# Performance work log

Hardware: AMD Instinct MI355X
Metric: run time of the kernel (lower is better)

## Reference

```python
import jax, jax.numpy as jnp
import numpy as np

E, S, L, V, PMAX = 256, 64, 3, 256, 2000
DILATIONS = (1, 2, 4, 8)


def _layernorm(x, g, b, eps=1e-5):
    m = x.mean(-1, keepdims=True)
    v = ((x - m) ** 2).mean(-1, keepdims=True)
    return (x - m) * jax.lax.rsqrt(v + eps) * g + b


def _ssm_layer(x, in_w, conv_w, conv_b, dt_w, A_log, D_param, B_w, C_w, out_w, ln_g, ln_b):
    # x: [B, T, D]
    Bsz, T, Dm = x.shape
    xr = x @ in_w.T                                  # [B,T,2D]
    x_in, x_res = xr[..., :Dm], xr[..., Dm:]
    # causal depthwise conv, kernel=4, left-pad 3 (== torch pad=3 then [:, :, :T])
    xt = x_in.transpose(0, 2, 1)                     # [B,D,T]
    xc = jax.lax.conv_general_dilated(
        xt, conv_w[:, None, :], (1,), [(3, 0)],
        feature_group_count=Dm, dimension_numbers=('NCH', 'OIH', 'NCH'))
    xc = jax.nn.silu((xc + conv_b[None, :, None]).transpose(0, 2, 1))  # [B,T,D]
    A = -jnp.exp(A_log)                              # [D,S]
    Bm = xc @ B_w.T                                  # [B,T,S]
    Cm = xc @ C_w.T                                  # [B,T,S]
    dt = jax.nn.softplus(dt_w)                       # [D] per-channel timestep
    dA = 1.0 + dt[:, None] * A                       # Euler discretization I + dt*A, [D,S]
    h0 = jnp.zeros((Bsz, Dm, S), x.dtype)

    def step(h, inp):
        u_t, B_t, C_t = inp                          # [B,D],[B,S],[B,S]
        h = dA * h + (dt * u_t)[:, :, None] * B_t[:, None, :]   # [B,D,S]
        y = jnp.einsum('bs,bds->bd', C_t, h)
        return h, y

    _, ys = jax.lax.scan(step, h0, (xc.transpose(1, 0, 2), Bm.transpose(1, 0, 2), Cm.transpose(1, 0, 2)))
    y = ys.transpose(1, 0, 2) + D_param * xc         # [B,T,D]
    y = (y * jax.nn.silu(x_res)) @ out_w.T
    return _layernorm(y + x, ln_g, ln_b)


def _forward(tokens, tok_emb, pos_emb, in_w, conv_w, conv_b, dt_w, A_log, D_param,
             B_w, C_w, out_w, ln_g, ln_b, ctx_w, ctx_b, fus_w, fus_b, fus_ln_g, fus_ln_b):
    Bsz, T = tokens.shape
    x = tok_emb[tokens] + pos_emb[:T][None]          # [B,T,E]
    feats = x
    for i in range(L):
        feats = _ssm_layer(feats, in_w[i], conv_w[i], conv_b[i], dt_w[i], A_log[i],
                           D_param[i], B_w[i], C_w[i], out_w[i], ln_g[i], ln_b[i])
    # multi-dilation context convs on the raw embeddings
    xt = x.transpose(0, 2, 1)                        # [B,E,T]
    ctx = []
    for j, d in enumerate(DILATIONS):
        o = jax.lax.conv_general_dilated(
            xt, ctx_w[j], (1,), [(d, d)], rhs_dilation=(d,),
            dimension_numbers=('NCH', 'OIH', 'NCH'))
        ctx.append(o + ctx_b[j][None, :, None])
    ctx = jnp.concatenate(ctx, axis=1).transpose(0, 2, 1)      # [B,T,E]
    fused = jax.nn.relu(jnp.concatenate([feats, ctx], -1) @ fus_w.T + fus_b)
    return _layernorm(fused, fus_ln_g, fus_ln_b)


def setup_inputs() -> dict:
    key = jax.random.key(0)
    ks = jax.random.split(key, 16)
    Bsz, T = 32, 2000

    def n(k, shape, s):
        return jax.random.normal(k, shape, jnp.float32) * s

    return {
        'tokens': jax.random.randint(ks[0], (Bsz, T), 0, V),
        'tok_emb': n(ks[1], (V, E), 1.0),
        'pos_emb': n(ks[2], (PMAX, E), 1.0),
        'in_w': n(ks[3], (L, 2 * E, E), 0.05),
        'conv_w': n(ks[4], (L, E, 4), 0.2),
        'conv_b': jnp.zeros((L, E), jnp.float32),
        'dt_w': jax.random.uniform(ks[5], (L, E), jnp.float32, -0.01, 0.01),
        'A_log': jax.random.uniform(ks[6], (L, E, S), jnp.float32, -4.0, -1.0),
        'D_param': jnp.zeros((L, E), jnp.float32),
        'B_w': n(ks[7], (L, S, E), 0.05),
        'C_w': n(ks[8], (L, S, E), 0.05),
        'out_w': n(ks[9], (L, E, E), 0.05),
        'ln_g': jnp.ones((L, E), jnp.float32),
        'ln_b': jnp.zeros((L, E), jnp.float32),
        'ctx_w': n(ks[10], (4, E // 4, E, 3), 0.05),
        'ctx_b': jnp.zeros((4, E // 4), jnp.float32),
        'fus_w': n(ks[11], (E, 2 * E), 0.05),
        'fus_b': jnp.zeros((E,), jnp.float32),
        'fus_ln_g': jnp.ones((E,), jnp.float32),
        'fus_ln_b': jnp.zeros((E,), jnp.float32),
    }


def reference(tokens, tok_emb, pos_emb, in_w, conv_w, conv_b, dt_w, A_log, D_param,
              B_w, C_w, out_w, ln_g, ln_b, ctx_w, ctx_b, fus_w, fus_b, fus_ln_g, fus_ln_b):
    return _forward(tokens, tok_emb, pos_emb, in_w, conv_w, conv_b, dt_w, A_log, D_param,
                    B_w, C_w, out_w, ln_g, ln_b, ctx_w, ctx_b, fus_w, fus_b, fus_ln_g, fus_ln_b)
```

## Files before the change

### kernel.cpp

```cpp
#include <hip/hip_runtime.h>
#include <stdint.h>

#define B_ 32
#define T_ 2000
#define E_ 256
#define S_ 64
#define L_ 3
#define BT_ (B_*T_)
#define NC_ 16
#define CL_ 125
#define TP_ (T_+16)

typedef short s8v __attribute__((ext_vector_type(8)));
typedef short s4v __attribute__((ext_vector_type(4)));
typedef float f4v __attribute__((ext_vector_type(4)));
typedef unsigned short us;

__device__ __forceinline__ float b2f(us u){
    return __uint_as_float(((unsigned int)u) << 16);
}
__device__ __forceinline__ us f2b(float f){
    unsigned int x = __float_as_uint(f);
    x += 0x7fffu + ((x >> 16) & 1u);
    return (us)(x >> 16);
}

__global__ __launch_bounds__(256) void cvtw_k(const float* __restrict__ src,
    us* __restrict__ dst)
{
    int idx = blockIdx.x*256 + threadIdx.x;
    f4v v = *(const f4v*)(src + (size_t)idx*4);
    s4v o;
    #pragma unroll
    for (int j=0;j<4;j++) o[j] = (short)f2b(v[j]);
    *(s4v*)(dst + (size_t)idx*4) = o;
}

__global__ __launch_bounds__(256) void packw_k(const float* __restrict__ cw,
    us* __restrict__ wp)
{
    int idx = blockIdx.x*256 + threadIdx.x;
    int i2 = idx % 768; int r = idx / 768;
    int c = r & 63; int j = r >> 6;
    int tap = i2 >> 8; int i = i2 & 255;
    wp[idx] = f2b(cw[(((size_t)(j*64 + c))*E_ + i)*3 + tap]);
}

__global__ __launch_bounds__(256) void embed_k(const int* __restrict__ tok,
    const float* __restrict__ te, const float* __restrict__ pe, us* __restrict__ x0)
{
    int idx = blockIdx.x*256 + threadIdx.x;
    int dg = idx & 31; int bt = idx >> 5; int t = bt % T_;
    int tk = tok[bt] & 255;
    const float* ta = te + (size_t)tk*E_ + dg*8;
    const float* pa = pe + (size_t)t*E_ + dg*8;
    f4v a0 = *(const f4v*)ta, a1 = *(const f4v*)(ta+4);
    f4v p0 = *(const f4v*)pa, p1 = *(const f4v*)(pa+4);
    s8v o;
    #pragma unroll
    for (int j=0;j<4;j++){
        o[j]   = (short)f2b(a0[j] + p0[j]);
        o[j+4] = (short)f2b(a1[j] + p1[j]);
    }
    *(s8v*)(x0 + (size_t)bt*E_ + dg*8) = o;
}

__global__ __launch_bounds__(256) void lconst_k(const float* __restrict__ dt_w,
    const float* __restrict__ A_log, float* __restrict__ dtv,
    float* __restrict__ dAT, float* __restrict__ dApT)
{
    int idx = blockIdx.x*256 + threadIdx.x;
    int d = idx & (E_-1); int s = idx >> 8;
    float dt = log1pf(expf(dt_w[d]));
    float A  = -expf(A_log[d*S_ + s]);
    float dA = 1.f + dt*A;
    dAT[s*E_ + d]  = dA;
    dApT[s*E_ + d] = powf(dA, (float)CL_);
    if (s == 0) dtv[d] = dt;
}

__global__ __launch_bounds__(256) void dwconv_k(const us* __restrict__ xin,
    const float* __restrict__ cw, const float* __restrict__ cb, us* __restrict__ xc)
{
    int idx = blockIdx.x*256 + threadIdx.x;
    int dg = idx & 31; int bt = idx >> 5; int t = bt % T_;
    int d0 = dg*8;
    float acc[8]; float w[8][4];
    #pragma unroll
    for (int j=0;j<8;j++){
        f4v wv = *(const f4v*)(cw + (size_t)(d0+j)*4);
        #pragma unroll
        for (int k=0;k<4;k++) w[j][k] = wv[k];
        acc[j] = cb[d0+j];
    }
    #pragma unroll
    for (int k=0;k<4;k++){
        if (t + k - 3 >= 0){
            s8v xv = *(const s8v*)(xin + (size_t)(bt + k - 3)*E_ + d0);
            #pragma unroll
            for (int j=0;j<8;j++) acc[j] = fmaf(b2f((us)xv[j]), w[j][k], acc[j]);
        }
    }
    s8v o;
    #pragma unroll
    for (int j=0;j<8;j++){ float v = acc[j]; v = v / (1.f + expf(-v)); o[j] = (short)f2b(v); }
    *(s8v*)(xc + (size_t)bt*E_ + d0) = o;
}

#define BM 128
#define BN 64
#define BK 32

template<int AMODE, int EPI>
__global__ __launch_bounds__(256)
void gemm_k(const us* __restrict__ A1, const us* __restrict__ A2,
            int lda, int shift,
            const us* __restrict__ W, int ldw,
            void* __restrict__ C1, const float* __restrict__ bias,
            int ldc, int K)
{
    __shared__ us Al[BM*BK];
    __shared__ us Bl[BN*BK];
    const int tid = threadIdx.x;
    const int wid = tid >> 6, lane = tid & 63;
    const int m0 = blockIdx.x * BM;
    const int n0 = blockIdx.y * BN;
    const int wr = wid >> 1, wc = wid & 1;
    f4v acc[4][2];
    #pragma unroll
    for (int a=0;a<4;a++)
        #pragma unroll
        for (int b=0;b<2;b++) acc[a][b] = (f4v){0.f,0.f,0.f,0.f};

    for (int k0 = 0; k0 < K; k0 += BK){
        s8v va[2], vb;
        #pragma unroll
        for (int i=0;i<2;i++){
            int g = i*256 + tid;
            int row = g >> 2, ks = g & 3;
            const us* src;
            if constexpr (AMODE==0){
                src = A1 + (size_t)(m0+row)*lda + k0 + ks*8;
            } else if constexpr (AMODE==2){
                int kk = k0 + ks*8;
                const us* base = (kk < E_) ? A1 : A2;
                src = base + (size_t)(m0+row)*E_ + (kk & (E_-1));
            } else {
                int kk = k0 + ks*8;
                int tap = kk >> 8; int kin = kk & (E_-1);
                int m = m0 + row; int bb = m / T_; int tt = m - bb*T_;
                src = A1 + ((size_t)bb*TP_ + 8 + tt + (tap-1)*shift)*E_ + kin;
            }
            va[i] = *(const s8v*)src;
        }
        {
            int row = tid >> 2, ks = tid & 3;
            vb = *(const s8v*)(W + (size_t)(n0+row)*ldw + k0 + ks*8);
        }
        if (k0) __syncthreads();
        #pragma unroll
        for (int i=0;i<2;i++) *(s8v*)(Al + (size_t)(i*256 + tid)*8) = va[i];
        *(s8v*)(Bl + (size_t)tid*8) = vb;
        __syncthreads();

        s8v af[4], bfr[2];
        #pragma unroll
        for (int mr=0;mr<4;mr++)
            af[mr] = *(const s8v*)(Al + ((size_t)(wr*64 + mr*16 + (lane&15))*4 + (lane>>4))*8);
        #pragma unroll
        for (int nr=0;nr<2;nr++)
            bfr[nr] = *(const s8v*)(Bl + ((size_t)(wc*32 + nr*16 + (lane&15))*4 + (lane>>4))*8);
        #pragma unroll
        for (int mr=0;mr<4;mr++)
            #pragma unroll
            for (int nr=0;nr<2;nr++)
                acc[mr][nr] = __builtin_amdgcn_mfma_f32_16x16x32_bf16(af[mr], bfr[nr], acc[mr][nr], 0, 0, 0);
    }
    #pragma unroll
    for (int mr=0;mr<4;mr++){
        #pragma unroll
        for (int nr=0;nr<2;nr++){
            int col = n0 + wc*32 + nr*16 + (lane & 15);
            int rb  = m0 + wr*64 + mr*16 + ((lane >> 4) << 2);
            #pragma unroll
            for (int i=0;i<4;i++){
                float val = acc[mr][nr][i];
                size_t row = (size_t)(rb + i);
                if constexpr (EPI==0){
                    ((us*)C1)[row*ldc + col] = f2b(val);
                } else if constexpr (EPI==5){
                    val += bias[col];
                    ((us*)C1)[row*ldc + col] = f2b(val);
                } else {
                    val += bias[col];
                    val = fmaxf(val, 0.f);
                    ((float*)C1)[row*ldc + col] = val;
                }
            }
        }
    }
}

__global__ __launch_bounds__(256) void scan_local(
    const float* __restrict__ dAT, const float* __restrict__ dtv,
    const us* __restrict__ xc, const us* __restrict__ Bm, const us* __restrict__ Cm,
    us* __restrict__ ys, us* __restrict__ H)
{
    int b = blockIdx.x >> 4, c = blockIdx.x & (NC_-1);
    int d = threadIdx.x;
    float h[S_], dAr[S_];
    #pragma unroll
    for (int s=0;s<S_;s++){ h[s]=0.f; dAr[s]=dAT[s*E_+d]; }
    float dtd = dtv[d];
    int t0 = c*CL_;
    for (int t=t0; t<t0+CL_; ++t){
        size_t bt = (size_t)b*T_ + t;
        float ku = dtd * b2f(xc[bt*E_ + d]);
        const s8v* Bp = (const s8v*)(Bm + bt*S_);
        const s8v* Cp = (const s8v*)(Cm + bt*S_);
        float y = 0.f;
        #pragma unroll
        for (int s8=0;s8<S_/8;s8++){
            s8v bv = Bp[s8], cv = Cp[s8];
            #pragma unroll
            for (int j=0;j<8;j++){
                int s = s8*8+j;
                h[s] = fmaf(dAr[s], h[s], ku*b2f((us)bv[j]));
                y    = fmaf(b2f((us)cv[j]), h[s], y);
            }
        }
        ys[bt*E_ + d] = f2b(y);
    }
    size_t hb = ((size_t)(b*NC_ + c))*S_*E_ + d;
    #pragma unroll
    for (int s=0;s<S_;s++) H[hb + (size_t)s*E_] = f2b(h[s]);
}

__global__ __launch_bounds__(256) void carry_k(const float* __restrict__ dApT,
    us* H)
{
    int idx = blockIdx.x*256 + threadIdx.x;
    int d = idx & (E_-1); int s = (idx >> 8) & (S_-1); int b = idx >> 14;
    float ap = dApT[s*E_ + d];
    size_t base = ((size_t)(b*NC_))*S_*E_ + (size_t)s*E_ + d;
    float hh = 0.f;
    for (int c=0;c<NC_;c++){
        size_t p = base + (size_t)c*S_*E_;
        float hl = b2f(H[p]);
        H[p] = f2b(hh);
        hh = fmaf(ap, hh, hl);
    }
}

__global__ __launch_bounds__(256) void scan_fix(
    const float* __restrict__ dAT, const us* __restrict__ H,
    const us* __restrict__ Cm, us* ys)
{
    int b = blockIdx.x / (NC_-1); int c = 1 + blockIdx.x % (NC_-1);
    int d = threadIdx.x;
    float w[S_], dAr[S_];
    size_t cb = ((size_t)(b*NC_ + c))*S_*E_ + d;
    #pragma unroll
    for (int s=0;s<S_;s++){ dAr[s] = dAT[s*E_+d]; w[s] = dAr[s]*b2f(H[cb + (size_t)s*E_]); }
    int t0 = c*CL_;
    for (int t=t0; t<t0+CL_; ++t){
        size_t bt = (size_t)b*T_ + t;
        const s8v* Cp = (const s8v*)(Cm + bt*S_);
        float y = 0.f;
        #pragma unroll
        for (int s8=0;s8<S_/8;s8++){
            s8v cv = Cp[s8];
            #pragma unroll
            for (int j=0;j<8;j++){
                int s = s8*8+j;
                y = fmaf(b2f((us)cv[j]), w[s], y);
                w[s] *= dAr[s];
            }
        }
        size_t p = bt*E_ + d;
        ys[p] = f2b(b2f(ys[p]) + y);
    }
}

__global__ __launch_bounds__(256) void zin_k(const us* __restrict__ ys,
    const us* xc, const us* __restrict__ xres,
    const float* __restrict__ Dp, us* zout)
{
    size_t e0 = ((size_t)blockIdx.x*256 + threadIdx.x)*4;
    int d0 = (int)(e0 & (E_-1));
    s4v yv  = *(const s4v*)(ys + e0);
    s4v xcv = *(const s4v*)(xc + e0);
    s4v xrv = *(const s4v*)(xres + e0);
    f4v dv  = *(const f4v*)(Dp + d0);
    s4v o;
    #pragma unroll
    for (int j=0;j<4;j++){
        float y  = b2f((us)yv[j]) + dv[j] * b2f((us)xcv[j]);
        float xr = b2f((us)xrv[j]);
        o[j] = (short)f2b(y * (xr / (1.f + expf(-xr))));
    }
    *(s4v*)(zout + e0) = o;
}

__global__ __launch_bounds__(256) void ln_k(const us* z,
    const us* __restrict__ resid, const float* __restrict__ g,
    const float* __restrict__ bb, us* out)
{
    int wid = threadIdx.x >> 6, lane = threadIdx.x & 63;
    size_t row = (size_t)blockIdx.x*4 + wid;
    size_t base = row*E_ + lane*4;
    s4v zv = *(const s4v*)(z + base);
    float v[4];
    #pragma unroll
    for (int j=0;j<4;j++) v[j] = b2f((us)zv[j]);
    if (resid){
        s4v rv = *(const s4v*)(resid + base);
        #pragma unroll
        for (int j=0;j<4;j++) v[j] += b2f((us)rv[j]);
    }
    float sum = v[0]+v[1]+v[2]+v[3];
    float sq  = v[0]*v[0]+v[1]*v[1]+v[2]*v[2]+v[3]*v[3];
    #pragma unroll
    for (int off=32; off>0; off>>=1){
        sum += __shfl_xor(sum, off, 64);
        sq  += __shfl_xor(sq,  off, 64);
    }
    float mean = sum * (1.f/E_);
    float var  = sq * (1.f/E_) - mean*mean;
    float rstd = rsqrtf(var + 1e-5f);
    f4v gv = *(const f4v*)(g + lane*4);
    f4v bv = *(const f4v*)(bb + lane*4);
    s4v o;
    #pragma unroll
    for (int j=0;j<4;j++)
        o[j] = (short)f2b((v[j]-mean)*rstd*gv[j] + bv[j]);
    *(s4v*)(out + base) = o;
}

__global__ __launch_bounds__(256) void ln_f32_k(const float* z,
    const float* __restrict__ g, const float* __restrict__ bb, float* out)
{
    int wid = threadIdx.x >> 6, lane = threadIdx.x & 63;
    size_t row = (size_t)blockIdx.x*4 + wid;
    size_t base = row*E_ + lane*4;
    f4v v = *(const f4v*)(z + base);
    float sum = v[0]+v[1]+v[2]+v[3];
    float sq  = v[0]*v[0]+v[1]*v[1]+v[2]*v[2]+v[3]*v[3];
    #pragma unroll
    for (int off=32; off>0; off>>=1){
        sum += __shfl_xor(sum, off, 64);
        sq  += __shfl_xor(sq,  off, 64);
    }
    float mean = sum * (1.f/E_);
    float var  = sq * (1.f/E_) - mean*mean;
    float rstd = rsqrtf(var + 1e-5f);
    f4v gv = *(const f4v*)(g + lane*4);
    f4v bv = *(const f4v*)(bb + lane*4);
    f4v o;
    #pragma unroll
    for (int j=0;j<4;j++)
        o[j] = (v[j]-mean)*rstd*gv[j] + bv[j];
    *(f4v*)(out + base) = o;
}

__global__ __launch_bounds__(256) void xpad_k(const us* __restrict__ x0,
    us* __restrict__ xp)
{
    int idx = blockIdx.x*256 + threadIdx.x;
    int dg = idx & 31; int r = idx >> 5;
    int tp = r % TP_; int b = r / TP_;
    s8v o;
    if (tp < 8 || tp >= T_+8){
        #pragma unroll
        for (int j=0;j<8;j++) o[j] = 0;
    } else {
        o = *(const s8v*)(x0 + ((size_t)b*T_ + tp - 8)*E_ + dg*8);
    }
    *(s8v*)(xp + (size_t)r*E_ + dg*8) = o;
}

__global__ void probe_k(const unsigned int* __restrict__ outw,
    const us* p0, const us* bm, const us* ctxb, const us* p1, const us* xc,
    const float* temb, float* outf)
{
    if (threadIdx.x | blockIdx.x) return;
    bool zero = true;
    for (int i=0;i<512 && zero;i++)              if (outw[i]) zero = false;
    for (int i=2000000;i<2000512 && zero;i++)    if (outw[i]) zero = false;
    if (!zero) return;
    int code = 256, f;
    f=0; for (int i=0;i<256;i++) if (p0[i]   & 0x7FFF) f=1;  code += 128*f;
    f=0; for (int i=0;i<256;i++) if (bm[i]   & 0x7FFF) f=1;  code += 64*f;
    f=0; for (int i=0;i<256;i++) if (ctxb[i] & 0x7FFF) f=1;  code += 32*f;
    f=0; for (int i=0;i<256;i++) if (p1[i]   & 0x7FFF) f=1;  code += 16*f;
    f=0; for (int i=0;i<256;i++) if (xc[i]   & 0x7FFF) f=1;  code += 8*f;
    f=1; for (int i=0;i<64;i++){ float v = fabsf(temb[i]); if (!(v < 1024.f)) f=0; }
    code += 4*f;
    outf[0] = (float)code;
}

extern "C" void kernel_launch(void* const* d_in, const int* in_sizes, int n_in,
                              void* d_out, int out_size, void* d_ws, size_t ws_size,
                              hipStream_t stream)
{
    const int*   tokens   = (const int*)d_in[0];
    const float* tok_emb  = (const float*)d_in[1];
    const float* pos_emb  = (const float*)d_in[2];
    const float* in_w     = (const float*)d_in[3];
    const float* conv_w   = (const float*)d_in[4];
    const float* conv_b   = (const float*)d_in[5];
    const float* dt_w     = (const float*)d_in[6];
    const float* A_log    = (const float*)d_in[7];
    const float* D_param  = (const float*)d_in[8];
    const float* B_w      = (const float*)d_in[9];
    const float* C_w      = (const float*)d_in[10];
    const float* out_w    = (const float*)d_in[11];
    const float* ln_g     = (const float*)d_in[12];
    const float* ln_b     = (const float*)d_in[13];
    const float* ctx_w    = (const float*)d_in[14];
    const float* ctx_b    = (const float*)d_in[15];
    const float* fus_w    = (const float*)d_in[16];
    const float* fus_b    = (const float*)d_in[17];
    const float* fus_ln_g = (const float*)d_in[18];
    const float* fus_ln_b = (const float*)d_in[19];

    char* ws = (char*)d_ws;
    size_t off = 0;
    auto alloc = [&](size_t bytes){ size_t o = off; off += (bytes + 255) & ~(size_t)255; return o; };
    const size_t BT = BT_;
    size_t o_p0  = alloc(BT*E_*2);
    size_t o_p1  = alloc(BT*E_*2);
    size_t o_ctx = alloc(BT*E_*2);
    size_t o_xin = alloc(BT*E_*2);
    size_t o_xc  = alloc(BT*E_*2);
    size_t o_bm  = alloc(BT*S_*2);
    size_t o_cm  = alloc(BT*S_*2);
    size_t o_h   = alloc((size_t)B_*NC_*S_*E_*2);
    size_t o_wp  = alloc((size_t)4*64*768*2);
    size_t o_wi  = alloc((size_t)L_*2*E_*E_*2);
    size_t o_wo  = alloc((size_t)L_*E_*E_*2);
    size_t o_wb  = alloc((size_t)L_*S_*E_*2);
    size_t o_wc  = alloc((size_t)L_*S_*E_*2);
    size_t o_wf  = alloc((size_t)E_*2*E_*2);
    size_t o_dtv = alloc(E_*4);
    size_t o_dat = alloc(E_*S_*4);
    size_t o_dap = alloc(E_*S_*4);
    (void)ws_size; (void)in_sizes; (void)n_in; (void)out_size;

    us* P0   = (us*)(ws + o_p0);
    us* P1   = (us*)(ws + o_p1);
    us* CTXB = (us*)(ws + o_ctx);
    us* XIN  = (us*)(ws + o_xin);
    us* XC   = (us*)(ws + o_xc);
    us* Bm   = (us*)(ws + o_bm);
    us* Cm   = (us*)(ws + o_cm);
    us* Hb   = (us*)(ws + o_h);
    us* WP   = (us*)(ws + o_wp);
    us* WI   = (us*)(ws + o_wi);
    us* WO   = (us*)(ws + o_wo);
    us* WB   = (us*)(ws + o_wb);
    us* WC   = (us*)(ws + o_wc);
    us* WF   = (us*)(ws + o_wf);
    float* DTV  = (float*)(ws + o_dtv);
    float* DAT  = (float*)(ws + o_dat);
    float* DAPT = (float*)(ws + o_dap);
    us* XPAD = XIN;
    us* YS   = (us*)d_out;

    cvtw_k<<<L_*2*E_*E_/1024, 256, 0, stream>>>(in_w,  WI);
    cvtw_k<<<L_*E_*E_/1024,   256, 0, stream>>>(out_w, WO);
    cvtw_k<<<L_*S_*E_/1024,   256, 0, stream>>>(B_w,   WB);
    cvtw_k<<<L_*S_*E_/1024,   256, 0, stream>>>(C_w,   WC);
    cvtw_k<<<E_*2*E_/1024,    256, 0, stream>>>(fus_w, WF);
    packw_k<<<4*64*768/256,   256, 0, stream>>>(ctx_w, WP);

    embed_k<<<BT_*32/256, 256, 0, stream>>>(tokens, tok_emb, pos_emb, P0);

    xpad_k<<<B_*TP_*32/256, 256, 0, stream>>>(P0, XPAD);
    const int dil[4] = {1,2,4,8};
    for (int j = 0; j < 4; ++j){
        gemm_k<3,5><<<dim3(BT_/BM, 1), 256, 0, stream>>>(
            XPAD, nullptr, E_, dil[j], WP + (size_t)j*64*768, 768,
            CTXB + j*64, ctx_b + j*64, E_, 768);
    }

    for (int l = 0; l < L_; ++l){
        const us* xprev = (l==1) ? P1 : P0;
        us*       xnext = (l==1) ? P0 : P1;

        lconst_k<<<E_*S_/256, 256, 0, stream>>>(dt_w + (size_t)l*E_, A_log + (size_t)l*E_*S_,
                                                DTV, DAT, DAPT);
        gemm_k<0,0><<<dim3(BT_/BM, E_/BN), 256, 0, stream>>>(
            xprev, nullptr, E_, 0, WI + (size_t)l*2*E_*E_, E_, XIN, nullptr, E_, E_);
        dwconv_k<<<BT_*32/256, 256, 0, stream>>>(XIN, conv_w + (size_t)l*E_*4, conv_b + (size_t)l*E_, XC);
        gemm_k<0,0><<<dim3(BT_/BM, E_/BN), 256, 0, stream>>>(
            xprev, nullptr, E_, 0, WI + (size_t)l*2*E_*E_ + (size_t)E_*E_, E_, XIN , nullptr, E_, E_);
        gemm_k<0,0><<<dim3(BT_/BM, 1), 256, 0, stream>>>(
            XC, nullptr, E_, 0, WB + (size_t)l*S_*E_, E_, Bm, nullptr, S_, E_);
        gemm_k<0,0><<<dim3(BT_/BM, 1), 256, 0, stream>>>(
            XC, nullptr, E_, 0, WC + (size_t)l*S_*E_, E_, Cm, nullptr, S_, E_);
        scan_local<<<B_*NC_, 256, 0, stream>>>(DAT, DTV, XC, Bm, Cm, YS, Hb);
        carry_k<<<B_*S_*E_/256, 256, 0, stream>>>(DAPT, Hb);
        scan_fix<<<B_*(NC_-1), 256, 0, stream>>>(DAT, Hb, Cm, YS);
        zin_k<<<BT_*E_/4/256, 256, 0, stream>>>(YS, XC, XIN, D_param + (size_t)l*E_, XC );
        gemm_k<0,0><<<dim3(BT_/BM, E_/BN), 256, 0, stream>>>(
            XC, nullptr, E_, 0, WO + (size_t)l*E_*E_, E_, XIN , nullptr, E_, E_);
        ln_k<<<BT_/4, 256, 0, stream>>>(XIN, xprev, ln_g + (size_t)l*E_, ln_b + (size_t)l*E_, xnext);
    }

    gemm_k<2,6><<<dim3(BT_/BM, E_/BN), 256, 0, stream>>>(
        P1, CTXB, E_, 0, WF, 2*E_, d_out, fus_b, E_, 2*E_);
    ln_f32_k<<<BT_/4, 256, 0, stream>>>((const float*)d_out, fus_ln_g, fus_ln_b, (float*)d_out);

    probe_k<<<1, 64, 0, stream>>>((const unsigned int*)d_out, P0, Bm, CTXB, P1, XC,
                                  tok_emb, (float*)d_out);
}
```

Baseline: 1.475 ms.

## Split SSM scan state across four lanes per channel and store B/C in fp32

The chunked scan kernels now give each channel four threads, each holding 16 of the 64 state entries, and combine partial outputs with lane shuffles. This launches four times as many blocks and cuts per-thread register arrays from 128 to 32 floats, aiming for higher occupancy in the sequential scan. The B and C projection GEMMs now write fp32 instead of bf16, which removes unpacking in the scan but doubles their memory traffic. The probe kernel is trimmed to match the changed buffers.

New measurement: 2.823 ms. +91.4%, slower.

```diff
diff --git a/kernel.cpp b/kernel.cpp
--- a/kernel.cpp
+++ b/kernel.cpp
@@ -188,6 +188,8 @@
                 size_t row = (size_t)(rb + i);
                 if constexpr (EPI==0){
                     ((us*)C1)[row*ldc + col] = f2b(val);
+                } else if constexpr (EPI==2){
+                    ((float*)C1)[row*ldc + col] = val;
                 } else if constexpr (EPI==5){
                     val += bias[col];
                     ((us*)C1)[row*ldc + col] = f2b(val);
@@ -203,37 +205,45 @@
 
 __global__ __launch_bounds__(256) void scan_local(
     const float* __restrict__ dAT, const float* __restrict__ dtv,
-    const us* __restrict__ xc, const us* __restrict__ Bm, const us* __restrict__ Cm,
+    const us* __restrict__ xc, const float* __restrict__ Bm, const float* __restrict__ Cm,
     us* __restrict__ ys, us* __restrict__ H)
 {
-    int b = blockIdx.x >> 4, c = blockIdx.x & (NC_-1);
-    int d = threadIdx.x;
-    float h[S_], dAr[S_];
-    #pragma unroll
-    for (int s=0;s<S_;s++){ h[s]=0.f; dAr[s]=dAT[s*E_+d]; }
+    int blk = blockIdx.x;
+    int dq = blk & 3;
+    int c  = (blk >> 2) & (NC_-1);
+    int b  = blk >> 6;
+    int tid = threadIdx.x;
+    int dl = tid >> 2, sg = tid & 3;
+    int d  = dq*64 + dl;
+    int s0 = sg*16;
+    float h[16], dAr[16];
+    #pragma unroll
+    for (int j=0;j<16;j++){ h[j]=0.f; dAr[j]=dAT[(s0+j)*E_ + d]; }
     float dtd = dtv[d];
     int t0 = c*CL_;
     for (int t=t0; t<t0+CL_; ++t){
         size_t bt = (size_t)b*T_ + t;
-        float ku = dtd * b2f(xc[bt*E_ + d]);
-        const s8v* Bp = (const s8v*)(Bm + bt*S_);
-        const s8v* Cp = (const s8v*)(Cm + bt*S_);
+        float u = dtd * b2f(xc[bt*E_ + d]);
+        const f4v* Bp = (const f4v*)(Bm + bt*S_ + s0);
+        const f4v* Cp = (const f4v*)(Cm + bt*S_ + s0);
         float y = 0.f;
         #pragma unroll
-        for (int s8=0;s8<S_/8;s8++){
-            s8v bv = Bp[s8], cv = Cp[s8];
+        for (int q=0;q<4;q++){
+            f4v bv = Bp[q], cv = Cp[q];
             #pragma unroll
-            for (int j=0;j<8;j++){
-                int s = s8*8+j;
-                h[s] = fmaf(dAr[s], h[s], ku*b2f((us)bv[j]));
-                y    = fmaf(b2f((us)cv[j]), h[s], y);
+            for (int j=0;j<4;j++){
+                int s = q*4+j;
+                h[s] = fmaf(dAr[s], h[s], u*bv[j]);
+                y    = fmaf(cv[j], h[s], y);
             }
         }
-        ys[bt*E_ + d] = f2b(y);
+        y += __shfl_xor(y, 1, 64);
+        y += __shfl_xor(y, 2, 64);
+        if (sg == 0) ys[bt*E_ + d] = f2b(y);
     }
     size_t hb = ((size_t)(b*NC_ + c))*S_*E_ + d;
     #pragma unroll
-    for (int s=0;s<S_;s++) H[hb + (size_t)s*E_] = f2b(h[s]);
+    for (int j=0;j<16;j++) H[hb + (size_t)(s0+j)*E_] = f2b(h[j]);
 }
 
 __global__ __launch_bounds__(256) void carry_k(const float* __restrict__ dApT,
@@ -254,31 +264,45 @@
 
 __global__ __launch_bounds__(256) void scan_fix(
     const float* __restrict__ dAT, const us* __restrict__ H,
-    const us* __restrict__ Cm, us* ys)
-{
-    int b = blockIdx.x / (NC_-1); int c = 1 + blockIdx.x % (NC_-1);
-    int d = threadIdx.x;
-    float w[S_], dAr[S_];
+    const float* __restrict__ Cm, us* ys)
+{
+    int blk = blockIdx.x;
+    int dq = blk & 3;
+    int r  = blk >> 2;
+    int c  = 1 + r % (NC_-1);
+    int b  = r / (NC_-1);
+    int tid = threadIdx.x;
+    int dl = tid >> 2, sg = tid & 3;
+    int d  = dq*64 + dl;
+    int s0 = sg*16;
+    float w[16], dAr[16];
     size_t cb = ((size_t)(b*NC_ + c))*S_*E_ + d;
     #pragma unroll
-    for (int s=0;s<S_;s++){ dAr[s] = dAT[s*E_+d]; w[s] = dAr[s]*b2f(H[cb + (size_t)s*E_]); }
+    for (int j=0;j<16;j++){
+        dAr[j] = dAT[(s0+j)*E_ + d];
+        w[j]   = dAr[j]*b2f(H[cb + (size_t)(s0+j)*E_]);
+    }
     int t0 = c*CL_;
     for (int t=t0; t<t0+CL_; ++t){
         size_t bt = (size_t)b*T_ + t;
-        const s8v* Cp = (const s8v*)(Cm + bt*S_);
+        const f4v* Cp = (const f4v*)(Cm + bt*S_ + s0);
         float y = 0.f;
         #pragma unroll
-        for (int s8=0;s8<S_/8;s8++){
-            s8v cv = Cp[s8];
+        for (int q=0;q<4;q++){
+            f4v cv = Cp[q];
             #pragma unroll
-            for (int j=0;j<8;j++){
-                int s = s8*8+j;
-                y = fmaf(b2f((us)cv[j]), w[s], y);
+            for (int j=0;j<4;j++){
+                int s = q*4+j;
+                y = fmaf(cv[j], w[s], y);
                 w[s] *= dAr[s];
             }
         }
-        size_t p = bt*E_ + d;
-        ys[p] = f2b(b2f(ys[p]) + y);
+        y += __shfl_xor(y, 1, 64);
+        y += __shfl_xor(y, 2, 64);
+        if (sg == 0){
+            size_t p = bt*E_ + d;
+            ys[p] = f2b(b2f(ys[p]) + y);
+        }
     }
 }
 
@@ -380,8 +404,7 @@
 }
 
 __global__ void probe_k(const unsigned int* __restrict__ outw,
-    const us* p0, const us* bm, const us* ctxb, const us* p1, const us* xc,
-    const float* temb, float* outf)
+    const us* p0, const us* p1, float* outf)
 {
     if (threadIdx.x | blockIdx.x) return;
     bool zero = true;
@@ -389,13 +412,8 @@
     for (int i=2000000;i<2000512 && zero;i++)    if (outw[i]) zero = false;
     if (!zero) return;
     int code = 256, f;
-    f=0; for (int i=0;i<256;i++) if (p0[i]   & 0x7FFF) f=1;  code += 128*f;
-    f=0; for (int i=0;i<256;i++) if (bm[i]   & 0x7FFF) f=1;  code += 64*f;
-    f=0; for (int i=0;i<256;i++) if (ctxb[i] & 0x7FFF) f=1;  code += 32*f;
-    f=0; for (int i=0;i<256;i++) if (p1[i]   & 0x7FFF) f=1;  code += 16*f;
-    f=0; for (int i=0;i<256;i++) if (xc[i]   & 0x7FFF) f=1;  code += 8*f;
-    f=1; for (int i=0;i<64;i++){ float v = fabsf(temb[i]); if (!(v < 1024.f)) f=0; }
-    code += 4*f;
+    f=0; for (int i=0;i<256;i++) if (p0[i] & 0x7FFF) f=1;  code += 128*f;
+    f=0; for (int i=0;i<256;i++) if (p1[i] & 0x7FFF) f=1;  code += 16*f;
     outf[0] = (float)code;
 }
 
@@ -433,8 +451,8 @@
     size_t o_ctx = alloc(BT*E_*2);
     size_t o_xin = alloc(BT*E_*2);
     size_t o_xc  = alloc(BT*E_*2);
-    size_t o_bm  = alloc(BT*S_*2);
-    size_t o_cm  = alloc(BT*S_*2);
+    size_t o_bm  = alloc(BT*S_*4);
+    size_t o_cm  = alloc(BT*S_*4);
     size_t o_h   = alloc((size_t)B_*NC_*S_*E_*2);
     size_t o_wp  = alloc((size_t)4*64*768*2);
     size_t o_wi  = alloc((size_t)L_*2*E_*E_*2);
@@ -452,8 +470,8 @@
     us* CTXB = (us*)(ws + o_ctx);
     us* XIN  = (us*)(ws + o_xin);
     us* XC   = (us*)(ws + o_xc);
-    us* Bm   = (us*)(ws + o_bm);
-    us* Cm   = (us*)(ws + o_cm);
+    float* BmF = (float*)(ws + o_bm);
+    float* CmF = (float*)(ws + o_cm);
     us* Hb   = (us*)(ws + o_h);
     us* WP   = (us*)(ws + o_wp);
     us* WI   = (us*)(ws + o_wi);
@@ -495,13 +513,13 @@
         dwconv_k<<<BT_*32/256, 256, 0, stream>>>(XIN, conv_w + (size_t)l*E_*4, conv_b + (size_t)l*E_, XC);
         gemm_k<0,0><<<dim3(BT_/BM, E_/BN), 256, 0, stream>>>(
             xprev, nullptr, E_, 0, WI + (size_t)l*2*E_*E_ + (size_t)E_*E_, E_, XIN , nullptr, E_, E_);
-        gemm_k<0,0><<<dim3(BT_/BM, 1), 256, 0, stream>>>(
-            XC, nullptr, E_, 0, WB + (size_t)l*S_*E_, E_, Bm, nullptr, S_, E_);
-        gemm_k<0,0><<<dim3(BT_/BM, 1), 256, 0, stream>>>(
-            XC, nullptr, E_, 0, WC + (size_t)l*S_*E_, E_, Cm, nullptr, S_, E_);
-        scan_local<<<B_*NC_, 256, 0, stream>>>(DAT, DTV, XC, Bm, Cm, YS, Hb);
+        gemm_k<0,2><<<dim3(BT_/BM, 1), 256, 0, stream>>>(
+            XC, nullptr, E_, 0, WB + (size_t)l*S_*E_, E_, BmF, nullptr, S_, E_);
+        gemm_k<0,2><<<dim3(BT_/BM, 1), 256, 0, stream>>>(
+            XC, nullptr, E_, 0, WC + (size_t)l*S_*E_, E_, CmF, nullptr, S_, E_);
+        scan_local<<<B_*NC_*4, 256, 0, stream>>>(DAT, DTV, XC, BmF, CmF, YS, Hb);
         carry_k<<<B_*S_*E_/256, 256, 0, stream>>>(DAPT, Hb);
-        scan_fix<<<B_*(NC_-1), 256, 0, stream>>>(DAT, Hb, Cm, YS);
+        scan_fix<<<B_*(NC_-1)*4, 256, 0, stream>>>(DAT, Hb, CmF, YS);
         zin_k<<<BT_*E_/4/256, 256, 0, stream>>>(YS, XC, XIN, D_param + (size_t)l*E_, XC );
         gemm_k<0,0><<<dim3(BT_/BM, E_/BN), 256, 0, stream>>>(
             XC, nullptr, E_, 0, WO + (size_t)l*E_*E_, E_, XIN , nullptr, E_, E_);
@@ -512,6 +530,5 @@
         P1, CTXB, E_, 0, WF, 2*E_, d_out, fus_b, E_, 2*E_);
     ln_f32_k<<<BT_/4, 256, 0, stream>>>((const float*)d_out, fus_ln_g, fus_ln_b, (float*)d_out);
 
-    probe_k<<<1, 64, 0, stream>>>((const unsigned int*)d_out, P0, Bm, CTXB, P1, XC,
-                                  tok_emb, (float*)d_out);
-}
+    probe_k<<<1, 64, 0, stream>>>((const unsigned int*)d_out, P0, P1, (float*)d_out);
+}
```

## Fuse B/C projections into one fp32 GEMM and split scan into more chunks

Applied to the files above, without the earlier changes.

Packs B_w and C_w into one weight matrix so a single GEMM produces both projections, written as fp32 in an interleaved [BT,128] layout. The chunked scan now uses 40 chunks of 50 steps instead of 16 of 125, exposing more blocks for the serial scan kernels. The scan kernels read fp32 B/C directly, removing bf16 unpacking and one rounding step. In exchange, B/C storage doubles in size and the carry pass walks more chunks serially.

Measured after the change: 1.440 ms. 1.02x faster.

```diff
diff --git a/kernel.cpp b/kernel.cpp
--- a/kernel.cpp
+++ b/kernel.cpp
@@ -7,8 +7,8 @@
 #define S_ 64
 #define L_ 3
 #define BT_ (B_*T_)
-#define NC_ 16
-#define CL_ 125
+#define NC_ 40
+#define CL_ 50
 #define TP_ (T_+16)
 
 typedef short s8v __attribute__((ext_vector_type(8)));
@@ -34,6 +34,16 @@
     #pragma unroll
     for (int j=0;j<4;j++) o[j] = (short)f2b(v[j]);
     *(s4v*)(dst + (size_t)idx*4) = o;
+}
+
+__global__ __launch_bounds__(256) void packbc_k(const float* __restrict__ Bw,
+    const float* __restrict__ Cw, us* __restrict__ wbc)
+{
+    int idx = blockIdx.x*256 + threadIdx.x;
+    int i = idx & 255; int r = (idx >> 8) & 127; int l = idx >> 15;
+    const float* src = (r < 64) ? (Bw + ((size_t)l*S_ + r)*E_ + i)
+                                : (Cw + ((size_t)l*S_ + (r-64))*E_ + i);
+    wbc[idx] = f2b(*src);
 }
 
 __global__ __launch_bounds__(256) void packw_k(const float* __restrict__ cw,
@@ -188,6 +198,8 @@
                 size_t row = (size_t)(rb + i);
                 if constexpr (EPI==0){
                     ((us*)C1)[row*ldc + col] = f2b(val);
+                } else if constexpr (EPI==2){
+                    ((float*)C1)[row*ldc + col] = val;
                 } else if constexpr (EPI==5){
                     val += bias[col];
                     ((us*)C1)[row*ldc + col] = f2b(val);
@@ -203,10 +215,10 @@
 
 __global__ __launch_bounds__(256) void scan_local(
     const float* __restrict__ dAT, const float* __restrict__ dtv,
-    const us* __restrict__ xc, const us* __restrict__ Bm, const us* __restrict__ Cm,
+    const us* __restrict__ xc, const float* __restrict__ BC,
     us* __restrict__ ys, us* __restrict__ H)
 {
-    int b = blockIdx.x >> 4, c = blockIdx.x & (NC_-1);
+    int b = blockIdx.x / NC_, c = blockIdx.x % NC_;
     int d = threadIdx.x;
     float h[S_], dAr[S_];
     #pragma unroll
@@ -215,18 +227,18 @@
     int t0 = c*CL_;
     for (int t=t0; t<t0+CL_; ++t){
         size_t bt = (size_t)b*T_ + t;
-        float ku = dtd * b2f(xc[bt*E_ + d]);
-        const s8v* Bp = (const s8v*)(Bm + bt*S_);
-        const s8v* Cp = (const s8v*)(Cm + bt*S_);
+        float u = dtd * b2f(xc[bt*E_ + d]);
+        const f4v* Bp = (const f4v*)(BC + bt*128);
+        const f4v* Cp = Bp + 16;
         float y = 0.f;
         #pragma unroll
-        for (int s8=0;s8<S_/8;s8++){
-            s8v bv = Bp[s8], cv = Cp[s8];
+        for (int q=0;q<16;q++){
+            f4v bv = Bp[q], cv = Cp[q];
             #pragma unroll
-            for (int j=0;j<8;j++){
-                int s = s8*8+j;
-                h[s] = fmaf(dAr[s], h[s], ku*b2f((us)bv[j]));
-                y    = fmaf(b2f((us)cv[j]), h[s], y);
+            for (int j=0;j<4;j++){
+                int s = q*4+j;
+                h[s] = fmaf(dAr[s], h[s], u*bv[j]);
+                y    = fmaf(cv[j], h[s], y);
             }
         }
         ys[bt*E_ + d] = f2b(y);
@@ -254,7 +266,7 @@
 
 __global__ __launch_bounds__(256) void scan_fix(
     const float* __restrict__ dAT, const us* __restrict__ H,
-    const us* __restrict__ Cm, us* ys)
+    const float* __restrict__ BC, us* ys)
 {
     int b = blockIdx.x / (NC_-1); int c = 1 + blockIdx.x % (NC_-1);
     int d = threadIdx.x;
@@ -265,15 +277,15 @@
     int t0 = c*CL_;
     for (int t=t0; t<t0+CL_; ++t){
         size_t bt = (size_t)b*T_ + t;
-        const s8v* Cp = (const s8v*)(Cm + bt*S_);
+        const f4v* Cp = (const f4v*)(BC + bt*128) + 16;
         float y = 0.f;
         #pragma unroll
-        for (int s8=0;s8<S_/8;s8++){
-            s8v cv = Cp[s8];
+        for (int q=0;q<16;q++){
+            f4v cv = Cp[q];
             #pragma unroll
-            for (int j=0;j<8;j++){
-                int s = s8*8+j;
-                y = fmaf(b2f((us)cv[j]), w[s], y);
+            for (int j=0;j<4;j++){
+                int s = q*4+j;
+                y = fmaf(cv[j], w[s], y);
                 w[s] *= dAr[s];
             }
         }
@@ -380,8 +392,7 @@
 }
 
 __global__ void probe_k(const unsigned int* __restrict__ outw,
-    const us* p0, const us* bm, const us* ctxb, const us* p1, const us* xc,
-    const float* temb, float* outf)
+    const us* p0, const us* p1, float* outf)
 {
     if (threadIdx.x | blockIdx.x) return;
     bool zero = true;
@@ -389,13 +400,8 @@
     for (int i=2000000;i<2000512 && zero;i++)    if (outw[i]) zero = false;
     if (!zero) return;
     int code = 256, f;
-    f=0; for (int i=0;i<256;i++) if (p0[i]   & 0x7FFF) f=1;  code += 128*f;
-    f=0; for (int i=0;i<256;i++) if (bm[i]   & 0x7FFF) f=1;  code += 64*f;
-    f=0; for (int i=0;i<256;i++) if (ctxb[i] & 0x7FFF) f=1;  code += 32*f;
-    f=0; for (int i=0;i<256;i++) if (p1[i]   & 0x7FFF) f=1;  code += 16*f;
-    f=0; for (int i=0;i<256;i++) if (xc[i]   & 0x7FFF) f=1;  code += 8*f;
-    f=1; for (int i=0;i<64;i++){ float v = fabsf(temb[i]); if (!(v < 1024.f)) f=0; }
-    code += 4*f;
+    f=0; for (int i=0;i<256;i++) if (p0[i] & 0x7FFF) f=1;  code += 128*f;
+    f=0; for (int i=0;i<256;i++) if (p1[i] & 0x7FFF) f=1;  code += 16*f;
     outf[0] = (float)code;
 }
 
@@ -433,14 +439,12 @@
     size_t o_ctx = alloc(BT*E_*2);
     size_t o_xin = alloc(BT*E_*2);
     size_t o_xc  = alloc(BT*E_*2);
-    size_t o_bm  = alloc(BT*S_*2);
-    size_t o_cm  = alloc(BT*S_*2);
+    size_t o_bc  = alloc(BT*128*4);
     size_t o_h   = alloc((size_t)B_*NC_*S_*E_*2);
     size_t o_wp  = alloc((size_t)4*64*768*2);
     size_t o_wi  = alloc((size_t)L_*2*E_*E_*2);
     size_t o_wo  = alloc((size_t)L_*E_*E_*2);
-    size_t o_wb  = alloc((size_t)L_*S_*E_*2);
-    size_t o_wc  = alloc((size_t)L_*S_*E_*2);
+    size_t o_wbc = alloc((size_t)L_*128*E_*2);
     size_t o_wf  = alloc((size_t)E_*2*E_*2);
     size_t o_dtv = alloc(E_*4);
     size_t o_dat = alloc(E_*S_*4);
@@ -452,14 +456,12 @@
     us* CTXB = (us*)(ws + o_ctx);
     us* XIN  = (us*)(ws + o_xin);
     us* XC   = (us*)(ws + o_xc);
-    us* Bm   = (us*)(ws + o_bm);
-    us* Cm   = (us*)(ws + o_cm);
+    float* BCf = (float*)(ws + o_bc);
     us* Hb   = (us*)(ws + o_h);
     us* WP   = (us*)(ws + o_wp);
     us* WI   = (us*)(ws + o_wi);
     us* WO   = (us*)(ws + o_wo);
-    us* WB   = (us*)(ws + o_wb);
-    us* WC   = (us*)(ws + o_wc);
+    us* WBC  = (us*)(ws + o_wbc);
     us* WF   = (us*)(ws + o_wf);
     float* DTV  = (float*)(ws + o_dtv);
     float* DAT  = (float*)(ws + o_dat);
@@ -469,9 +471,8 @@
 
     cvtw_k<<<L_*2*E_*E_/1024, 256, 0, stream>>>(in_w,  WI);
     cvtw_k<<<L_*E_*E_/1024,   256, 0, stream>>>(out_w, WO);
-    cvtw_k<<<L_*S_*E_/1024,   256, 0, stream>>>(B_w,   WB);
-    cvtw_k<<<L_*S_*E_/1024,   256, 0, stream>>>(C_w,   WC);
     cvtw_k<<<E_*2*E_/1024,    256, 0, stream>>>(fus_w, WF);
+    packbc_k<<<L_*128*E_/256, 256, 0, stream>>>(B_w, C_w, WBC);
     packw_k<<<4*64*768/256,   256, 0, stream>>>(ctx_w, WP);
 
     embed_k<<<BT_*32/256, 256, 0, stream>>>(tokens, tok_emb, pos_emb, P0);
@@ -495,13 +496,11 @@
         dwconv_k<<<BT_*32/256, 256, 0, stream>>>(XIN, conv_w + (size_t)l*E_*4, conv_b + (size_t)l*E_, XC);
         gemm_k<0,0><<<dim3(BT_/BM, E_/BN), 256, 0, stream>>>(
             xprev, nullptr, E_, 0, WI + (size_t)l*2*E_*E_ + (size_t)E_*E_, E_, XIN , nullptr, E_, E_);
-        gemm_k<0,0><<<dim3(BT_/BM, 1), 256, 0, stream>>>(
-            XC, nullptr, E_, 0, WB + (size_t)l*S_*E_, E_, Bm, nullptr, S_, E_);
-        gemm_k<0,0><<<dim3(BT_/BM, 1), 256, 0, stream>>>(
-            XC, nullptr, E_, 0, WC + (size_t)l*S_*E_, E_, Cm, nullptr, S_, E_);
-        scan_local<<<B_*NC_, 256, 0, stream>>>(DAT, DTV, XC, Bm, Cm, YS, Hb);
+        gemm_k<0,2><<<dim3(BT_/BM, 2), 256, 0, stream>>>(
+            XC, nullptr, E_, 0, WBC + (size_t)l*128*E_, E_, BCf, nullptr, 128, E_);
+        scan_local<<<B_*NC_, 256, 0, stream>>>(DAT, DTV, XC, BCf, YS, Hb);
         carry_k<<<B_*S_*E_/256, 256, 0, stream>>>(DAPT, Hb);
-        scan_fix<<<B_*(NC_-1), 256, 0, stream>>>(DAT, Hb, Cm, YS);
+        scan_fix<<<B_*(NC_-1), 256, 0, stream>>>(DAT, Hb, BCf, YS);
         zin_k<<<BT_*E_/4/256, 256, 0, stream>>>(YS, XC, XIN, D_param + (size_t)l*E_, XC );
         gemm_k<0,0><<<dim3(BT_/BM, E_/BN), 256, 0, stream>>>(
             XC, nullptr, E_, 0, WO + (size_t)l*E_*E_, E_, XIN , nullptr, E_, E_);
@@ -512,6 +511,5 @@
         P1, CTXB, E_, 0, WF, 2*E_, d_out, fus_b, E_, 2*E_);
     ln_f32_k<<<BT_/4, 256, 0, stream>>>((const float*)d_out, fus_ln_g, fus_ln_b, (float*)d_out);
 
-    probe_k<<<1, 64, 0, stream>>>((const unsigned int*)d_out, P0, Bm, CTXB, P1, XC,
-                                  tok_emb, (float*)d_out);
-}
+    probe_k<<<1, 64, 0, stream>>>((const unsigned int*)d_out, P0, P1, (float*)d_out);
+}
```
